# Performance work log

Hardware: AMD Instinct MI355X
Metric: run time of the kernel (lower is better)

Reference implementation:

```python
import jax, jax.numpy as jnp
import numpy as np

BN, N, FIN, FO, H = 4, 2048, 128, 64, 4
D = FO * H  # 256


def setup_inputs() -> dict:
    key = jax.random.key(0)
    ks = jax.random.split(key, 13)
    rnd = lambda k, s, sc=1.0: jax.random.normal(k, s, dtype=jnp.float32) * sc
    return {
        "x": rnd(ks[0], (BN, N, FIN)),
        "adj": rnd(ks[1], (BN, N, N)),
        "W_proj": rnd(ks[2], (D, FIN), 0.08),        # xavier-ish scale
        "score_src": rnd(ks[3], (H, FO), 0.1),        # (head_num, out_features)
        "score_tgt": rnd(ks[4], (H, FO), 0.1),
        "bias_out": jnp.zeros((D,), jnp.float32),
        "w_r": rnd(ks[5], (D, D), 0.06),
        "u_r": rnd(ks[6], (D, D), 0.06),
        "w_z": rnd(ks[7], (D, D), 0.06),
        "b_wz": jnp.full((D,), -2.0, jnp.float32),    # GRUGate init_bias
        "u_z": rnd(ks[8], (D, D), 0.06),
        "w_g": rnd(ks[9], (D, D), 0.06),
        "u_g": rnd(ks[10], (D, D), 0.06),
    }


def reference(x, adj, W_proj, score_src, score_tgt, bias_out,
              w_r, u_r, w_z, b_wz, u_z, w_g, u_g):
    bn, n = x.shape[:2]
    h, fo = score_src.shape
    # eval mode: dropout is identity
    proj_flat = x @ W_proj.T                                   # (bn, n, fo*h)
    # reshape splits last dim as (fo, h): head index fastest-varying
    proj = proj_flat.reshape(bn, n, fo, h).transpose(0, 3, 1, 2)  # (bn, h, n, fo)
    residual = proj_flat                                       # (bn, n, fo*h)
    s_src = jnp.einsum('bhnf,hf->bhn', proj, score_src)
    s_tgt = jnp.einsum('bhnf,hf->bhn', proj, score_tgt)
    scores = jax.nn.leaky_relu(s_src[..., :, None] + s_tgt[..., None, :], 0.2)
    scores = scores + adj[:, None]                             # (bn, h, n, n)
    attn = jax.nn.softmax(scores, axis=-1)
    out = jnp.einsum('bhij,bhjf->bhif', attn, proj)            # (bn, h, n, fo)
    out = out.transpose(0, 2, 1, 3).reshape(bn, n, h * fo)
    # GRUGate is computed in the torch source but its result is discarded
    z = jax.nn.sigmoid(out @ w_z.T + b_wz + residual @ u_z.T)
    r = jax.nn.sigmoid(out @ w_r.T + residual @ u_r.T)
    h_hat = jnp.tanh(out @ w_g.T + (r * residual) @ u_g.T)
    _gru = (1.0 - z) * residual + z * h_hat  # unused, matches source bug
    return jax.nn.elu(out + bias_out)
```

## Files before the change

### kernel.cpp

```cpp
#include <hip/hip_runtime.h>
#include <hip/hip_bf16.h>
#include <math.h>

#define BN_   4
#define NN_   2048
#define FIN_  128
#define FO_   64
#define H_    4
#define D_    256

typedef __attribute__((ext_vector_type(8))) short bf16x8;
typedef __attribute__((ext_vector_type(4))) float floatx4;

#define LOG2E 1.4426950408889634f

#if __has_builtin(__builtin_amdgcn_exp2f)
#define EXP2(x) __builtin_amdgcn_exp2f(x)
#else
#define EXP2(x) exp2f(x)
#endif

__device__ __forceinline__ float bf2f(short u) {
    union { unsigned int i; float f; } v;
    v.i = ((unsigned int)(unsigned short)u) << 16;
    return v.f;
}
__device__ __forceinline__ short f2bf(float f) {
    union { float f; unsigned int u; } v; v.f = f;
    unsigned int r = v.u + 0x7fffu + ((v.u >> 16) & 1u);
    return (short)(unsigned short)(r >> 16);
}

#if defined(__BF16_MANT_DIG__)
typedef __bf16 bfr2 __attribute__((ext_vector_type(2)));
__device__ __forceinline__ unsigned int pack_bf16(float a, float b) {
    union { bfr2 h; unsigned int u; } v;
    v.h = (bfr2){(__bf16)a, (__bf16)b};
    return v.u;
}
#else
__device__ __forceinline__ unsigned int pack_bf16(float a, float b) {
    return ((unsigned int)(unsigned short)f2bf(a)) |
           (((unsigned int)(unsigned short)f2bf(b)) << 16);
}
#endif

__device__ __forceinline__ bf16x8 load8f(const float* __restrict__ p) {
    floatx4 a = *(const floatx4*)p;
    floatx4 b = *(const floatx4*)(p + 4);
    union { bf16x8 v; unsigned int u[4]; } r;
    r.u[0] = pack_bf16(a[0], a[1]);
    r.u[1] = pack_bf16(a[2], a[3]);
    r.u[2] = pack_bf16(b[0], b[1]);
    r.u[3] = pack_bf16(b[2], b[3]);
    return r.v;
}

__device__ __forceinline__ float score_exp(float ssv, float stv, float av) {
    float s = ssv + stv;
    s = fmaxf(s, 0.2f * s);
    return EXP2((s + av) * LOG2E);
}

__global__ __launch_bounds__(256) void proj_kernel(
    const float* __restrict__ x,
    const float* __restrict__ wproj,
    const float* __restrict__ ssrc,
    const float* __restrict__ stgt,
    short* __restrict__ pt,
    float* __restrict__ sS,
    float* __restrict__ sT,
    int b0)
{
    __shared__ short ptl[64][264];

    const int tid  = threadIdx.x;
    const int wave = tid >> 6;
    const int lane = tid & 63;
    const int l16  = lane & 15;
    const int quad = lane >> 4;

    const int b_rel = blockIdx.z;
    const int b  = b0 + b_rel;
    const int h  = blockIdx.y;
    const int j0 = blockIdx.x * 256 + wave * 64;

    floatx4 acc[4][4];
#pragma unroll
    for (int mi = 0; mi < 4; ++mi)
#pragma unroll
        for (int nj = 0; nj < 4; ++nj)
            acc[mi][nj] = (floatx4){0.f, 0.f, 0.f, 0.f};

#pragma unroll
    for (int kc = 0; kc < 4; ++kc) {
        const int c = kc * 32 + quad * 8;
        bf16x8 afr[4], bfr[4];
#pragma unroll
        for (int mi = 0; mi < 4; ++mi) {
            int f = mi * 16 + l16;
            int srow = f * H_ + h;
            afr[mi] = load8f(wproj + srow * FIN_ + c);
        }
#pragma unroll
        for (int nj = 0; nj < 4; ++nj) {
            int j = j0 + nj * 16 + l16;
            bfr[nj] = load8f(x + ((size_t)b * NN_ + j) * FIN_ + c);
        }
#pragma unroll
        for (int mi = 0; mi < 4; ++mi)
#pragma unroll
            for (int nj = 0; nj < 4; ++nj)
                acc[mi][nj] = __builtin_amdgcn_mfma_f32_16x16x32_bf16(
                    afr[mi], bfr[nj], acc[mi][nj], 0, 0, 0);
    }

#pragma unroll
    for (int mi = 0; mi < 4; ++mi)
#pragma unroll
        for (int r = 0; r < 4; ++r)
#pragma unroll
            for (int nj = 0; nj < 4; ++nj)
                ptl[mi * 16 + quad * 4 + r][wave * 64 + nj * 16 + l16] =
                    f2bf(acc[mi][nj][r]);

    float wsv[4][4], wtv[4][4];
#pragma unroll
    for (int mi = 0; mi < 4; ++mi)
#pragma unroll
        for (int r = 0; r < 4; ++r) {
            int f = mi * 16 + quad * 4 + r;
            wsv[mi][r] = ssrc[h * FO_ + f];
            wtv[mi][r] = stgt[h * FO_ + f];
        }
    const size_t sbase = ((size_t)b_rel * H_ + h) * NN_;
#pragma unroll
    for (int nj = 0; nj < 4; ++nj) {
        float ps = 0.f, pg = 0.f;
#pragma unroll
        for (int mi = 0; mi < 4; ++mi)
#pragma unroll
            for (int r = 0; r < 4; ++r) {
                ps = fmaf(wsv[mi][r], acc[mi][nj][r], ps);
                pg = fmaf(wtv[mi][r], acc[mi][nj][r], pg);
            }
        ps += __shfl_xor(ps, 16, 64); ps += __shfl_xor(ps, 32, 64);
        pg += __shfl_xor(pg, 16, 64); pg += __shfl_xor(pg, 32, 64);
        if (quad == 0) {
            int j = j0 + nj * 16 + l16;
            sS[sbase + j] = ps;
            sT[sbase + j] = pg;
        }
    }

    __syncthreads();

    const size_t base = ((size_t)b_rel * H_ + h) * (size_t)(64 * 2048)
                      + (size_t)(blockIdx.x * 8) * 2048;
#pragma unroll
    for (int p = 0; p < 8; ++p) {
        const int uid  = p * 256 + tid;
        const int mi   = (uid >> 6) & 3;
        const int l    = uid & 63;
        const int tile = uid >> 8;
        const int f    = mi * 16 + (l & 15);
        const int js   = tile * 32 + (l >> 4) * 8;
        bf16x8 v = *(const bf16x8*)&ptl[f][js];
        *(bf16x8*)&pt[base + (size_t)uid * 8] = v;
    }
}

#define RSTRIDE 65
#define WSLOT   (RSTRIDE * 16 + 16)

__global__ __launch_bounds__(512, 2) void attn_kernel(
    const float* __restrict__ adj,
    const short* __restrict__ pt,
    const float* __restrict__ sS,
    const float* __restrict__ sT,
    const float* __restrict__ bias,
    float* __restrict__ out,
    int b0)
{
    __shared__ union {
        struct {
            float adjs[8][16][36];
            float st[8][4][256];
        } m;
        float red[8][WSLOT];
    } sm;

    const int tid  = threadIdx.x;
    const int w    = tid >> 6;
    const int lane = tid & 63;
    const int l16  = lane & 15;
    const int quad = lane >> 4;
    const int r8   = lane >> 3;
    const int c4   = (lane & 7) * 4;

    int bx = blockIdx.x, bz = blockIdx.z;
    if (gridDim.z == 4 && gridDim.x == 128) {
        const int flat = bx + 128 * bz;
        const int xcd  = flat & 7;
        bz = xcd >> 1;
        bx = (xcd & 1) * 64 + (flat >> 3);
    }
    const int b_rel = bz;
    const int b  = b0 + b_rel;
    const int i0 = bx * 16;

    const short* pt2_b = pt + (size_t)b_rel * H_ * (size_t)(64 * 2048);
    const size_t sb = (size_t)b_rel * H_ * NN_;

    {
        const int t = lane * 4;
#pragma unroll
        for (int h = 0; h < 4; ++h)
            *(floatx4*)&sm.m.st[w][h][t] =
                *(const floatx4*)&sT[sb + (size_t)h * NN_ + w * 256 + t];
    }

    float ssv[4];
#pragma unroll
    for (int h = 0; h < 4; ++h)
        ssv[h] = sS[sb + (size_t)h * NN_ + i0 + l16];

    const float* adj_base = adj + ((size_t)b * NN_ + i0) * NN_ + w * 256;

    floatx4 acc[4][4];
#pragma unroll
    for (int h = 0; h < 4; ++h)
#pragma unroll
        for (int K = 0; K < 4; ++K)
            acc[h][K] = (floatx4){0.f, 0.f, 0.f, 0.f};
    float ls[4] = {0.f, 0.f, 0.f, 0.f};

    floatx4 areg0 = *(const floatx4*)(adj_base + (size_t)r8 * NN_ + c4);
    floatx4 areg1 = *(const floatx4*)(adj_base + (size_t)(8 + r8) * NN_ + c4);
    *(floatx4*)&sm.m.adjs[w][r8][c4]     = areg0;
    *(floatx4*)&sm.m.adjs[w][8 + r8][c4] = areg1;

    const int lo8 = lane * 8;

#pragma unroll
    for (int jt = 0; jt < 8; ++jt) {
        const int o  = jt * 32;
        const int qo = quad * 8;

        if (jt < 7) {
            areg0 = *(const floatx4*)(adj_base + (size_t)r8 * NN_ + o + 32 + c4);
            areg1 = *(const floatx4*)(adj_base + (size_t)(8 + r8) * NN_ + o + 32 + c4);
        }

        floatx4 ajA = *(const floatx4*)&sm.m.adjs[w][l16][qo];
        floatx4 ajB = *(const floatx4*)&sm.m.adjs[w][l16][qo + 4];

#pragma unroll
        for (int u = 0; u < 4; ++u) {
            const short* fb = pt2_b + ((size_t)u * 64 + (w * 8 + jt)) * 2048 + lo8;
            bf16x8 bfr[4];
#pragma unroll
            for (int K = 0; K < 4; ++K)
                bfr[K] = *(const bf16x8*)(fb + K * 512);

            const float* stp = &sm.m.st[w][u][qo];
            floatx4 stA = *(const floatx4*)(stp + o);
            floatx4 stB = *(const floatx4*)(stp + o + 4);

            float w0 = score_exp(ssv[u], stA[0], ajA[0]);
            float w1 = score_exp(ssv[u], stA[1], ajA[1]);
            float w2 = score_exp(ssv[u], stA[2], ajA[2]);
            float w3 = score_exp(ssv[u], stA[3], ajA[3]);
            float w4 = score_exp(ssv[u], stB[0], ajB[0]);
            float w5 = score_exp(ssv[u], stB[1], ajB[1]);
            float w6 = score_exp(ssv[u], stB[2], ajB[2]);
            float w7 = score_exp(ssv[u], stB[3], ajB[3]);
            ls[u] += ((w0 + w1) + (w2 + w3)) + ((w4 + w5) + (w6 + w7));
            union { bf16x8 v; unsigned int u4[4]; } a0;
            a0.u4[0] = pack_bf16(w0, w1);
            a0.u4[1] = pack_bf16(w2, w3);
            a0.u4[2] = pack_bf16(w4, w5);
            a0.u4[3] = pack_bf16(w6, w7);
#pragma unroll
            for (int K = 0; K < 4; ++K)
                acc[u][K] = __builtin_amdgcn_mfma_f32_16x16x32_bf16(
                    a0.v, bfr[K], acc[u][K], 0, 0, 0);
        }

        if (jt < 7) {
            *(floatx4*)&sm.m.adjs[w][r8][c4]     = areg0;
            *(floatx4*)&sm.m.adjs[w][8 + r8][c4] = areg1;
        }
    }

#pragma unroll
    for (int h = 0; h < 4; ++h) {
        ls[h] += __shfl_xor(ls[h], 16, 64);
        ls[h] += __shfl_xor(ls[h], 32, 64);
    }

#pragma unroll
    for (int h = 0; h < 4; ++h) {
        __syncthreads();
#pragma unroll
        for (int K = 0; K < 4; ++K)
#pragma unroll
            for (int r = 0; r < 4; ++r)
                sm.red[w][(quad * 4 + r) * RSTRIDE + K * 16 + l16] = acc[h][K][r];
        if (quad == 0)
            sm.red[w][16 * RSTRIDE + l16] = ls[h];
        __syncthreads();
#pragma unroll
        for (int p = 0; p < 2; ++p) {
            int e   = tid + p * 512;
            int row = e >> 6;
            int col = e & 63;
            float s = 0.f, l = 0.f;
#pragma unroll
            for (int ww = 0; ww < 8; ++ww) {
                s += sm.red[ww][row * RSTRIDE + col];
                l += sm.red[ww][16 * RSTRIDE + row];
            }
            float v = s / l + bias[h * FO_ + col];
            v = (v > 0.f) ? v : expm1f(v);
            out[((size_t)b * NN_ + i0 + row) * D_ + h * FO_ + col] = v;
        }
    }
}

extern "C" void kernel_launch(void* const* d_in, const int* in_sizes, int n_in,
                              void* d_out, int out_size, void* d_ws, size_t ws_size,
                              hipStream_t stream) {
    const float* x     = (const float*)d_in[0];
    const float* adj   = (const float*)d_in[1];
    const float* wproj = (const float*)d_in[2];
    const float* ssrc  = (const float*)d_in[3];
    const float* stgt  = (const float*)d_in[4];
    const float* bias  = (const float*)d_in[5];
    float* out = (float*)d_out;

    const size_t SLAB  = (size_t)D_ * NN_ * 2;
    const size_t SSLAB = (size_t)2 * H_ * NN_ * 4;
    int nb = (int)(ws_size / (SLAB + SSLAB));
    if (nb < 1) nb = 1;
    if (nb > 4) nb = 4;

    short* pt = (short*)d_ws;
    float* sv = (float*)((char*)d_ws + (size_t)nb * SLAB);
    float* sS = sv;
    float* sT = sv + (size_t)nb * H_ * NN_;

    for (int bb0 = 0; bb0 < BN_; bb0 += nb) {
        int cnt = (BN_ - bb0 < nb) ? (BN_ - bb0) : nb;
        proj_kernel<<<dim3(NN_ / 256, H_, cnt), 256, 0, stream>>>(
            x, wproj, ssrc, stgt, pt, sS, sT, bb0);
        attn_kernel<<<dim3(NN_ / 16, 1, cnt), 512, 0, stream>>>(
            adj, pt, sS, sT, bias, out, bb0);
    }
}
```

Before: 163.1 us.

## Process 32 query rows per attention block to reuse projected feature loads

Each attention block now covers two 16-row sub-tiles (32 rows), so every bf16 projection fragment loaded from global memory feeds twice as many MFMAs. The grid is halved and the XCD remapping is adjusted to match. The cost is doubled accumulator registers (32 floatx4 per thread) and a larger adjacency staging buffer in shared memory. Under launch_bounds(512,2) this risks register spills, and it leaves fewer blocks to fill the GPU (256 blocks).

Measured after the change: 158.4 us (median of 2 runs). 1.03x faster.

```diff
diff --git a/kernel.cpp b/kernel.cpp
--- a/kernel.cpp
+++ b/kernel.cpp
@@ -184,7 +184,7 @@
 {
     __shared__ union {
         struct {
-            float adjs[8][16][36];
+            float adjs[8][32][36];
             float st[8][4][256];
         } m;
         float red[8][WSLOT];
@@ -199,15 +199,15 @@
     const int c4   = (lane & 7) * 4;
 
     int bx = blockIdx.x, bz = blockIdx.z;
-    if (gridDim.z == 4 && gridDim.x == 128) {
-        const int flat = bx + 128 * bz;
+    if (gridDim.z == 4 && gridDim.x == 64) {
+        const int flat = bx + 64 * bz;
         const int xcd  = flat & 7;
         bz = xcd >> 1;
-        bx = (xcd & 1) * 64 + (flat >> 3);
+        bx = (xcd & 1) * 32 + (flat >> 3);
     }
     const int b_rel = bz;
     const int b  = b0 + b_rel;
-    const int i0 = bx * 16;
+    const int i0 = bx * 32;
 
     const short* pt2_b = pt + (size_t)b_rel * H_ * (size_t)(64 * 2048);
     const size_t sb = (size_t)b_rel * H_ * NN_;
@@ -220,25 +220,33 @@
                 *(const floatx4*)&sT[sb + (size_t)h * NN_ + w * 256 + t];
     }
 
-    float ssv[4];
-#pragma unroll
-    for (int h = 0; h < 4; ++h)
-        ssv[h] = sS[sb + (size_t)h * NN_ + i0 + l16];
+    float ssv[2][4];
+#pragma unroll
+    for (int sub = 0; sub < 2; ++sub)
+#pragma unroll
+        for (int h = 0; h < 4; ++h)
+            ssv[sub][h] = sS[sb + (size_t)h * NN_ + i0 + sub * 16 + l16];
 
     const float* adj_base = adj + ((size_t)b * NN_ + i0) * NN_ + w * 256;
 
-    floatx4 acc[4][4];
-#pragma unroll
-    for (int h = 0; h < 4; ++h)
-#pragma unroll
-        for (int K = 0; K < 4; ++K)
-            acc[h][K] = (floatx4){0.f, 0.f, 0.f, 0.f};
-    float ls[4] = {0.f, 0.f, 0.f, 0.f};
-
-    floatx4 areg0 = *(const floatx4*)(adj_base + (size_t)r8 * NN_ + c4);
-    floatx4 areg1 = *(const floatx4*)(adj_base + (size_t)(8 + r8) * NN_ + c4);
-    *(floatx4*)&sm.m.adjs[w][r8][c4]     = areg0;
-    *(floatx4*)&sm.m.adjs[w][8 + r8][c4] = areg1;
+    floatx4 acc[2][4][4];
+#pragma unroll
+    for (int sub = 0; sub < 2; ++sub)
+#pragma unroll
+        for (int h = 0; h < 4; ++h)
+#pragma unroll
+            for (int K = 0; K < 4; ++K)
+                acc[sub][h][K] = (floatx4){0.f, 0.f, 0.f, 0.f};
+    float ls[2][4] = {{0.f, 0.f, 0.f, 0.f}, {0.f, 0.f, 0.f, 0.f}};
+
+    floatx4 ar0 = *(const floatx4*)(adj_base + (size_t)r8 * NN_ + c4);
+    floatx4 ar1 = *(const floatx4*)(adj_base + (size_t)(8 + r8) * NN_ + c4);
+    floatx4 ar2 = *(const floatx4*)(adj_base + (size_t)(16 + r8) * NN_ + c4);
+    floatx4 ar3 = *(const floatx4*)(adj_base + (size_t)(24 + r8) * NN_ + c4);
+    *(floatx4*)&sm.m.adjs[w][r8][c4]      = ar0;
+    *(floatx4*)&sm.m.adjs[w][8 + r8][c4]  = ar1;
+    *(floatx4*)&sm.m.adjs[w][16 + r8][c4] = ar2;
+    *(floatx4*)&sm.m.adjs[w][24 + r8][c4] = ar3;
 
     const int lo8 = lane * 8;
 
@@ -248,12 +256,18 @@
         const int qo = quad * 8;
 
         if (jt < 7) {
-            areg0 = *(const floatx4*)(adj_base + (size_t)r8 * NN_ + o + 32 + c4);
-            areg1 = *(const floatx4*)(adj_base + (size_t)(8 + r8) * NN_ + o + 32 + c4);
-        }
-
-        floatx4 ajA = *(const floatx4*)&sm.m.adjs[w][l16][qo];
-        floatx4 ajB = *(const floatx4*)&sm.m.adjs[w][l16][qo + 4];
+            ar0 = *(const floatx4*)(adj_base + (size_t)r8 * NN_ + o + 32 + c4);
+            ar1 = *(const floatx4*)(adj_base + (size_t)(8 + r8) * NN_ + o + 32 + c4);
+            ar2 = *(const floatx4*)(adj_base + (size_t)(16 + r8) * NN_ + o + 32 + c4);
+            ar3 = *(const floatx4*)(adj_base + (size_t)(24 + r8) * NN_ + o + 32 + c4);
+        }
+
+        floatx4 ajA[2], ajB[2];
+#pragma unroll
+        for (int sub = 0; sub < 2; ++sub) {
+            ajA[sub] = *(const floatx4*)&sm.m.adjs[w][sub * 16 + l16][qo];
+            ajB[sub] = *(const floatx4*)&sm.m.adjs[w][sub * 16 + l16][qo + 4];
+        }
 
 #pragma unroll
         for (int u = 0; u < 4; ++u) {
@@ -267,38 +281,48 @@
             floatx4 stA = *(const floatx4*)(stp + o);
             floatx4 stB = *(const floatx4*)(stp + o + 4);
 
-            float w0 = score_exp(ssv[u], stA[0], ajA[0]);
-            float w1 = score_exp(ssv[u], stA[1], ajA[1]);
-            float w2 = score_exp(ssv[u], stA[2], ajA[2]);
-            float w3 = score_exp(ssv[u], stA[3], ajA[3]);
-            float w4 = score_exp(ssv[u], stB[0], ajB[0]);
-            float w5 = score_exp(ssv[u], stB[1], ajB[1]);
-            float w6 = score_exp(ssv[u], stB[2], ajB[2]);
-            float w7 = score_exp(ssv[u], stB[3], ajB[3]);
-            ls[u] += ((w0 + w1) + (w2 + w3)) + ((w4 + w5) + (w6 + w7));
-            union { bf16x8 v; unsigned int u4[4]; } a0;
-            a0.u4[0] = pack_bf16(w0, w1);
-            a0.u4[1] = pack_bf16(w2, w3);
-            a0.u4[2] = pack_bf16(w4, w5);
-            a0.u4[3] = pack_bf16(w6, w7);
-#pragma unroll
-            for (int K = 0; K < 4; ++K)
-                acc[u][K] = __builtin_amdgcn_mfma_f32_16x16x32_bf16(
-                    a0.v, bfr[K], acc[u][K], 0, 0, 0);
+#pragma unroll
+            for (int sub = 0; sub < 2; ++sub) {
+                const float sv = ssv[sub][u];
+                float w0 = score_exp(sv, stA[0], ajA[sub][0]);
+                float w1 = score_exp(sv, stA[1], ajA[sub][1]);
+                float w2 = score_exp(sv, stA[2], ajA[sub][2]);
+                float w3 = score_exp(sv, stA[3], ajA[sub][3]);
+                float w4 = score_exp(sv, stB[0], ajB[sub][0]);
+                float w5 = score_exp(sv, stB[1], ajB[sub][1]);
+                float w6 = score_exp(sv, stB[2], ajB[sub][2]);
+                float w7 = score_exp(sv, stB[3], ajB[sub][3]);
+                ls[sub][u] += ((w0 + w1) + (w2 + w3)) + ((w4 + w5) + (w6 + w7));
+                union { bf16x8 v; unsigned int u4[4]; } a0;
+                a0.u4[0] = pack_bf16(w0, w1);
+                a0.u4[1] = pack_bf16(w2, w3);
+                a0.u4[2] = pack_bf16(w4, w5);
+                a0.u4[3] = pack_bf16(w6, w7);
+#pragma unroll
+                for (int K = 0; K < 4; ++K)
+                    acc[sub][u][K] = __builtin_amdgcn_mfma_f32_16x16x32_bf16(
+                        a0.v, bfr[K], acc[sub][u][K], 0, 0, 0);
+            }
         }
 
         if (jt < 7) {
-            *(floatx4*)&sm.m.adjs[w][r8][c4]     = areg0;
-            *(floatx4*)&sm.m.adjs[w][8 + r8][c4] = areg1;
-        }
-    }
-
-#pragma unroll
-    for (int h = 0; h < 4; ++h) {
-        ls[h] += __shfl_xor(ls[h], 16, 64);
-        ls[h] += __shfl_xor(ls[h], 32, 64);
-    }
-
+            *(floatx4*)&sm.m.adjs[w][r8][c4]      = ar0;
+            *(floatx4*)&sm.m.adjs[w][8 + r8][c4]  = ar1;
+            *(floatx4*)&sm.m.adjs[w][16 + r8][c4] = ar2;
+            *(floatx4*)&sm.m.adjs[w][24 + r8][c4] = ar3;
+        }
+    }
+
+#pragma unroll
+    for (int sub = 0; sub < 2; ++sub)
+#pragma unroll
+        for (int h = 0; h < 4; ++h) {
+            ls[sub][h] += __shfl_xor(ls[sub][h], 16, 64);
+            ls[sub][h] += __shfl_xor(ls[sub][h], 32, 64);
+        }
+
+#pragma unroll
+    for (int sub = 0; sub < 2; ++sub)
 #pragma unroll
     for (int h = 0; h < 4; ++h) {
         __syncthreads();
@@ -306,9 +330,9 @@
         for (int K = 0; K < 4; ++K)
 #pragma unroll
             for (int r = 0; r < 4; ++r)
-                sm.red[w][(quad * 4 + r) * RSTRIDE + K * 16 + l16] = acc[h][K][r];
+                sm.red[w][(quad * 4 + r) * RSTRIDE + K * 16 + l16] = acc[sub][h][K][r];
         if (quad == 0)
-            sm.red[w][16 * RSTRIDE + l16] = ls[h];
+            sm.red[w][16 * RSTRIDE + l16] = ls[sub][h];
         __syncthreads();
 #pragma unroll
         for (int p = 0; p < 2; ++p) {
@@ -323,7 +347,7 @@
             }
             float v = s / l + bias[h * FO_ + col];
             v = (v > 0.f) ? v : expm1f(v);
-            out[((size_t)b * NN_ + i0 + row) * D_ + h * FO_ + col] = v;
+            out[((size_t)b * NN_ + i0 + sub * 16 + row) * D_ + h * FO_ + col] = v;
         }
     }
 }
@@ -354,7 +378,7 @@
         int cnt = (BN_ - bb0 < nb) ? (BN_ - bb0) : nb;
         proj_kernel<<<dim3(NN_ / 256, H_, cnt), 256, 0, stream>>>(
             x, wproj, ssrc, stgt, pt, sS, sT, bb0);
-        attn_kernel<<<dim3(NN_ / 16, 1, cnt), 512, 0, stream>>>(
+        attn_kernel<<<dim3(NN_ / 32, 1, cnt), 512, 0, stream>>>(
             adj, pt, sS, sT, bias, out, bb0);
     }
 }
```
